# Optimization experiments

Hardware: AMD Instinct MI355X
Metric: run time of the kernel (lower is better)

## Reference

```python
import jax, jax.numpy as jnp
import numpy as np

L, BAT, A, B, D, NBITS = 2, 32, 64, 1024, 128, 1024
PADDING = 0


def setup_inputs() -> dict:
    key = jax.random.key(0)
    k1, k2, k3, k4, k5 = jax.random.split(key, 5)
    query_embed = jax.random.normal(k1, (L, BAT, A, D), dtype=jnp.float32)
    doc_embed = jax.random.normal(k2, (L, BAT, B, D), dtype=jnp.float32)
    query_tok = jax.random.randint(k3, (BAT, A), 0, 2)
    doc_tok = jax.random.randint(k4, (BAT, B), 0, 2)
    # LSH projection matrix: randn * sigma + mu with sigma=0.1, mu=0
    r = jax.random.normal(k5, (NBITS, D), dtype=jnp.float32) * 0.1
    return {"query_embed": query_embed, "doc_embed": doc_embed,
            "query_tok": query_tok, "doc_tok": doc_tok, "r": r}


def reference(query_embed, doc_embed, query_tok, doc_tok, r):
    d = r.shape[0]  # num_bits
    # sign-hash: (emb @ r.T > 0).float()  -> binary codes in {0,1}
    c1 = (jnp.einsum('lbad,kd->lbak', query_embed, r) > 0).astype(jnp.float32)  # [L,BAT,A,NBITS]
    c2 = (jnp.einsum('lbcd,kd->lbck', doc_embed, r) > 0).astype(jnp.float32)    # [L,BAT,B,NBITS]
    # Hamming distance via popcount identity: |u-v|_H = sum(u) + sum(v) - 2 u.v
    s1 = c1.sum(-1)  # [L,BAT,A]
    s2 = c2.sum(-1)  # [L,BAT,B]
    dot = jnp.einsum('lbak,lbck->lbac', c1, c2)  # [L,BAT,A,B]
    ham = s1[..., :, None] + s2[..., None, :] - 2.0 * dot
    sim = jnp.cos(jnp.pi / d * ham)  # [L,BAT,A,B]
    # zero out padded query / doc positions
    qmask = (query_tok == PADDING)[None, :, :, None]
    dmask = (doc_tok == PADDING)[None, :, None, :]
    sim = jnp.where(qmask | dmask, 0.0, sim)
    # torch.stack(simmat, dim=1) -> [BAT, L, A, B]
    return jnp.transpose(sim, (1, 0, 2, 3))
```

## Files before the change

kernel.cpp:

```cpp
#include <hip/hip_runtime.h>
#include <math.h>

#define L_ 2
#define BAT_ 32
#define A_ 64
#define B_ 1024
#define D_ 128
#define NBITS_ 1024
#define NW 32
#define NQROWS (L_*BAT_*A_)
#define NDROWS (L_*BAT_*B_)
#define NROWS (NQROWS + NDROWS)

#define TM 128
#define TN 128
#define KH 64
#define RS 136

typedef __bf16 bf16x4 __attribute__((ext_vector_type(4)));
typedef __bf16 bf16x8 __attribute__((ext_vector_type(8)));
typedef float  f32x4  __attribute__((ext_vector_type(4)));

__global__ __launch_bounds__(256) void hash_kernel(
    const float* __restrict__ qe, const float* __restrict__ de,
    const float* __restrict__ r, unsigned int* __restrict__ codes)
{
    __shared__ __align__(16) __bf16 As[TM * RS];
    __shared__ __align__(16) __bf16 Bs[TN * RS];

    const int t = threadIdx.x;
    const int row0 = blockIdx.x * TM;
    const int bit0 = blockIdx.y * TN;

    const float* abase = (row0 < NQROWS) ? (qe + (size_t)row0 * D_)
                                         : (de + (size_t)(row0 - NQROWS) * D_);
    const float* bbase = r + (size_t)bit0 * D_;

    const int wv   = t >> 6;
    const int lane = t & 63;
    const int quad = lane >> 4;
    const int col  = lane & 15;
    const int wrow = (wv >> 1) * 64;
    const int wbit = (wv & 1) * 64;

    f32x4 acc[4][4];
    #pragma unroll
    for (int ti = 0; ti < 4; ++ti)
        #pragma unroll
        for (int tj = 0; tj < 4; ++tj)
            acc[ti][tj] = (f32x4){0.f, 0.f, 0.f, 0.f};

    #pragma unroll
    for (int ks = 0; ks < D_; ks += KH) {
        if (ks) __syncthreads();
        #pragma unroll
        for (int i = 0; i < 8; ++i) {
            int f = (t + i * 256) * 4;
            int rr = f >> 6, cc = f & 63;
            float4 v = *(const float4*)(abase + (size_t)rr * D_ + ks + cc);
            bf16x4 hi, lo;
            hi[0] = (__bf16)v.x; hi[1] = (__bf16)v.y;
            hi[2] = (__bf16)v.z; hi[3] = (__bf16)v.w;
            lo[0] = (__bf16)(v.x - (float)hi[0]);
            lo[1] = (__bf16)(v.y - (float)hi[1]);
            lo[2] = (__bf16)(v.z - (float)hi[2]);
            lo[3] = (__bf16)(v.w - (float)hi[3]);
            *(bf16x4*)(&As[rr * RS + cc])      = hi;
            *(bf16x4*)(&As[rr * RS + 64 + cc]) = lo;
        }
        #pragma unroll
        for (int i = 0; i < 8; ++i) {
            int f = (t + i * 256) * 4;
            int rr = f >> 6, cc = f & 63;
            float4 v = *(const float4*)(bbase + (size_t)rr * D_ + ks + cc);
            bf16x4 hi, lo;
            hi[0] = (__bf16)v.x; hi[1] = (__bf16)v.y;
            hi[2] = (__bf16)v.z; hi[3] = (__bf16)v.w;
            lo[0] = (__bf16)(v.x - (float)hi[0]);
            lo[1] = (__bf16)(v.y - (float)hi[1]);
            lo[2] = (__bf16)(v.z - (float)hi[2]);
            lo[3] = (__bf16)(v.w - (float)hi[3]);
            *(bf16x4*)(&Bs[rr * RS + cc])      = hi;
            *(bf16x4*)(&Bs[rr * RS + 64 + cc]) = lo;
        }
        __syncthreads();

        #pragma unroll
        for (int seg = 0; seg < 3; ++seg) {
            const int ao = (seg == 2) ? 64 : 0;
            const int bo = (seg == 1) ? 64 : 0;
            #pragma unroll
            for (int kk = 0; kk < KH; kk += 32) {
                bf16x8 af[4], bfr[4];
                #pragma unroll
                for (int ti = 0; ti < 4; ++ti)
                    af[ti] = *(const bf16x8*)(
                        &As[(wrow + ti * 16 + col) * RS + ao + kk + quad * 8]);
                #pragma unroll
                for (int tj = 0; tj < 4; ++tj)
                    bfr[tj] = *(const bf16x8*)(
                        &Bs[(wbit + tj * 16 + col) * RS + bo + kk + quad * 8]);
                #pragma unroll
                for (int ti = 0; ti < 4; ++ti)
                    #pragma unroll
                    for (int tj = 0; tj < 4; ++tj)
                        acc[ti][tj] = __builtin_amdgcn_mfma_f32_16x16x32_bf16(
                            af[ti], bfr[tj], acc[ti][tj], 0, 0, 0);
            }
        }
    }

    #pragma unroll
    for (int ti = 0; ti < 4; ++ti) {
        #pragma unroll
        for (int rg = 0; rg < 4; ++rg) {
            unsigned long long b[4];
            #pragma unroll
            for (int tj = 0; tj < 4; ++tj)
                b[tj] = __ballot(acc[ti][tj][rg] > 0.f);
            if (col < 2) {
                const int w = col;
                unsigned int lo16 = (unsigned int)(b[2 * w]     >> (16 * quad)) & 0xFFFFu;
                unsigned int hi16 = (unsigned int)(b[2 * w + 1] >> (16 * quad)) & 0xFFFFu;
                const int row = row0 + wrow + ti * 16 + quad * 4 + rg;
                codes[(size_t)row * NW + (blockIdx.y * 4 + (wv & 1) * 2 + w)] =
                    lo16 | (hi16 << 16);
            }
        }
    }
}

__global__ __launch_bounds__(256) void simmat_kernel(
    const unsigned int* __restrict__ codes,
    const int* __restrict__ qtok, const int* __restrict__ dtok,
    float* __restrict__ out)
{
    __shared__ uint4 qc[8][8];
    __shared__ float lut[NBITS_ + 1];
    __shared__ float qm[8];

    const int blk  = blockIdx.x;
    const int ct   = blk & 3;
    const int asub = (blk >> 2) & 7;
    const int b    = (blk >> 5) & 31;
    const int l    = blk >> 10;
    const int t    = threadIdx.x;

    for (int h = t; h <= NBITS_; h += 256)
        lut[h] = cosf((float)M_PI / (float)NBITS_ * (float)h);

    const int a0 = asub * 8;
    const unsigned int* qbase =
        codes + (size_t)((l * BAT_ + b) * A_ + a0) * NW;
    if (t < 8 * NW) ((unsigned int*)qc)[t] = qbase[t];
    if (t < 8) qm[t] = (qtok[b * A_ + a0 + t] != 0) ? 1.f : 0.f;
    __syncthreads();

    const int c = ct * 256 + t;
    const unsigned int* dbase =
        codes + (size_t)(NQROWS + (l * BAT_ + b) * B_ + c) * NW;
    uint4 dc[8];
    #pragma unroll
    for (int w = 0; w < 8; ++w) dc[w] = *(const uint4*)(dbase + w * 4);
    const float dm = (dtok[b * B_ + c] != 0) ? 1.f : 0.f;

    float* obase = out + ((size_t)((b * L_ + l) * A_ + a0)) * B_ + c;
    #pragma unroll
    for (int ai = 0; ai < 8; ++ai) {
        int ham = 0;
        #pragma unroll
        for (int w = 0; w < 8; ++w) {
            uint4 qv = qc[ai][w];
            ham += __popc(qv.x ^ dc[w].x) + __popc(qv.y ^ dc[w].y)
                 + __popc(qv.z ^ dc[w].z) + __popc(qv.w ^ dc[w].w);
        }
        obase[(size_t)ai * B_] = lut[ham] * qm[ai] * dm;
    }
}

extern "C" void kernel_launch(void* const* d_in, const int* in_sizes, int n_in,
                              void* d_out, int out_size, void* d_ws, size_t ws_size,
                              hipStream_t stream) {
    const float* qe  = (const float*)d_in[0];
    const float* de  = (const float*)d_in[1];
    const int* qtok  = (const int*)d_in[2];
    const int* dtok  = (const int*)d_in[3];
    const float* r   = (const float*)d_in[4];
    float* out = (float*)d_out;
    unsigned int* codes = (unsigned int*)d_ws;

    dim3 g1(NROWS / TM, NBITS_ / TN);
    hash_kernel<<<g1, 256, 0, stream>>>(qe, de, r, codes);
    simmat_kernel<<<L_ * BAT_ * 4 * 8, 256, 0, stream>>>(codes, qtok, dtok, out);
}
```

Before: 177.5 us.

## Store hash codes word-major and process 32 queries per simmat block

The hash kernel now writes codes transposed (word-major across all rows), so each simmat thread's per-word loads of doc codes coalesce across threads instead of using strided 128-byte uint4 rows. The simmat kernel now handles 32 query rows per block instead of 8. This cuts the number of times doc codes are reloaded and the per-block LUT setup by 4x, and the query codes are staged in padded shared memory. In exchange the hash kernel's code stores become strided and scattered, simmat needs 32 registers for doc codes, and the grid shrinks to 512 blocks, which may reduce occupancy.

```diff
diff --git a/kernel.cpp b/kernel.cpp
--- a/kernel.cpp
+++ b/kernel.cpp
@@ -23,7 +23,7 @@
 
 __global__ __launch_bounds__(256) void hash_kernel(
     const float* __restrict__ qe, const float* __restrict__ de,
-    const float* __restrict__ r, unsigned int* __restrict__ codes)
+    const float* __restrict__ r, unsigned int* __restrict__ codes_t)
 {
     __shared__ __align__(16) __bf16 As[TM * RS];
     __shared__ __align__(16) __bf16 Bs[TN * RS];
@@ -123,58 +123,61 @@
                 unsigned int lo16 = (unsigned int)(b[2 * w]     >> (16 * quad)) & 0xFFFFu;
                 unsigned int hi16 = (unsigned int)(b[2 * w + 1] >> (16 * quad)) & 0xFFFFu;
                 const int row = row0 + wrow + ti * 16 + quad * 4 + rg;
-                codes[(size_t)row * NW + (blockIdx.y * 4 + (wv & 1) * 2 + w)] =
-                    lo16 | (hi16 << 16);
+                const int wg  = blockIdx.y * 4 + (wv & 1) * 2 + w;
+                codes_t[(size_t)wg * NROWS + row] = lo16 | (hi16 << 16);
             }
         }
     }
 }
 
 __global__ __launch_bounds__(256) void simmat_kernel(
-    const unsigned int* __restrict__ codes,
+    const unsigned int* __restrict__ codes_t,
     const int* __restrict__ qtok, const int* __restrict__ dtok,
     float* __restrict__ out)
 {
-    __shared__ uint4 qc[8][8];
+    __shared__ unsigned int qc[32 * 36];
     __shared__ float lut[NBITS_ + 1];
-    __shared__ float qm[8];
+    __shared__ float qm[32];
 
-    const int blk  = blockIdx.x;
-    const int ct   = blk & 3;
-    const int asub = (blk >> 2) & 7;
-    const int b    = (blk >> 5) & 31;
-    const int l    = blk >> 10;
-    const int t    = threadIdx.x;
+    const int blk = blockIdx.x;
+    const int ct  = blk & 3;
+    const int ah  = (blk >> 2) & 1;
+    const int b   = (blk >> 3) & 31;
+    const int l   = blk >> 8;
+    const int t   = threadIdx.x;
 
     for (int h = t; h <= NBITS_; h += 256)
         lut[h] = cosf((float)M_PI / (float)NBITS_ * (float)h);
 
-    const int a0 = asub * 8;
-    const unsigned int* qbase =
-        codes + (size_t)((l * BAT_ + b) * A_ + a0) * NW;
-    if (t < 8 * NW) ((unsigned int*)qc)[t] = qbase[t];
-    if (t < 8) qm[t] = (qtok[b * A_ + a0 + t] != 0) ? 1.f : 0.f;
+    const int a0 = ah * 32;
+    const int qrow0 = (l * BAT_ + b) * A_ + a0;
+    #pragma unroll
+    for (int i = 0; i < 4; ++i) {
+        int idx = i * 256 + t;
+        int w = idx >> 5, a = idx & 31;
+        qc[a * 36 + w] = codes_t[(size_t)w * NROWS + qrow0 + a];
+    }
+    if (t < 32) qm[t] = (qtok[b * A_ + a0 + t] != 0) ? 1.f : 0.f;
     __syncthreads();
 
     const int c = ct * 256 + t;
-    const unsigned int* dbase =
-        codes + (size_t)(NQROWS + (l * BAT_ + b) * B_ + c) * NW;
-    uint4 dc[8];
+    const size_t drow = (size_t)NQROWS + (size_t)(l * BAT_ + b) * B_ + c;
+    unsigned int dc[NW];
     #pragma unroll
-    for (int w = 0; w < 8; ++w) dc[w] = *(const uint4*)(dbase + w * 4);
+    for (int w = 0; w < NW; ++w) dc[w] = codes_t[(size_t)w * NROWS + drow];
     const float dm = (dtok[b * B_ + c] != 0) ? 1.f : 0.f;
 
     float* obase = out + ((size_t)((b * L_ + l) * A_ + a0)) * B_ + c;
-    #pragma unroll
-    for (int ai = 0; ai < 8; ++ai) {
+    #pragma unroll 4
+    for (int ai = 0; ai < 32; ++ai) {
         int ham = 0;
         #pragma unroll
-        for (int w = 0; w < 8; ++w) {
-            uint4 qv = qc[ai][w];
-            ham += __popc(qv.x ^ dc[w].x) + __popc(qv.y ^ dc[w].y)
-                 + __popc(qv.z ^ dc[w].z) + __popc(qv.w ^ dc[w].w);
+        for (int m = 0; m < 8; ++m) {
+            uint4 qv = *(const uint4*)(&qc[ai * 36 + m * 4]);
+            ham += __popc(qv.x ^ dc[4 * m])     + __popc(qv.y ^ dc[4 * m + 1])
+                 + __popc(qv.z ^ dc[4 * m + 2]) + __popc(qv.w ^ dc[4 * m + 3]);
         }
-        obase[(size_t)ai * B_] = lut[ham] * qm[ai] * dm;
+        obase[(size_t)ai * B_] = lut[ham] * (qm[ai] * dm);
     }
 }
 
@@ -187,9 +190,9 @@
     const int* dtok  = (const int*)d_in[3];
     const float* r   = (const float*)d_in[4];
     float* out = (float*)d_out;
-    unsigned int* codes = (unsigned int*)d_ws;
+    unsigned int* codes_t = (unsigned int*)d_ws;
 
     dim3 g1(NROWS / TM, NBITS_ / TN);
-    hash_kernel<<<g1, 256, 0, stream>>>(qe, de, r, codes);
-    simmat_kernel<<<L_ * BAT_ * 4 * 8, 256, 0, stream>>>(codes, qtok, dtok, out);
+    hash_kernel<<<g1, 256, 0, stream>>>(qe, de, r, codes_t);
+    simmat_kernel<<<L_ * BAT_ * 2 * 4, 256, 0, stream>>>(codes_t, qtok, dtok, out);
 }
```

Result: faster. 173.1 us (-2.5%).
